# Kernel tuning notes

Measured on AMD Instinct MI355X. Metric: run time of the kernel, lower is better.

The kernel has to match this reference:

```python
import jax, jax.numpy as jnp
import numpy as np


def _dft_mats(N1, N):
    # Symmetric N1xN1 DFT / iDFT matrices and Cooley-Tukey twiddle factors.
    n = np.arange(N1)
    F = np.exp(-2j * np.pi * np.outer(n, n) / N1).astype(np.complex64)
    Finv = np.conj(F)  # inverse DFT matrix (1/N normalization folded into tw)
    tw = (np.exp(-2j * np.pi * np.outer(n, n) / N) / N).astype(np.complex64)
    twinv = np.exp(2j * np.pi * np.outer(n, n) / N).astype(np.complex64)
    return F, Finv, tw, twinv


def setup_inputs() -> dict:
    key = jax.random.key(0)
    ku, kk = jax.random.split(key)
    B, H, N = 128, 128, 1024
    u = jax.random.normal(ku, (B, H, N), dtype=jnp.float32)
    k = jax.random.normal(kk, (H, N), dtype=jnp.float32)
    return {"u": u, "k": k}


def reference(u, k):
    # Four-step (Monarch / Cooley-Tukey) FFT convolution: y = ifft(fft(u) * fft(k)).real
    # decomposed into N1xN1 complex matmuls with twiddle multiplies, matching TKFFTConv.
    B, H, N = u.shape
    N1 = int(round(np.sqrt(N)))
    F, Finv, tw, twinv = map(jnp.asarray, _dft_mats(N1, N))

    # Filter spectrum, reshaped (k2, k1) then transposed -> (H, k1, k2), as in __init__.
    kf = jnp.fft.fft(k, n=N)                              # (H, N) complex64
    kfT = jnp.swapaxes(kf.reshape(H, N1, N1), -1, -2)     # (H, k1, k2)

    x = u.reshape(B, H, N1, N1).astype(jnp.complex64)     # (B, H, n1, n2)
    x = jnp.einsum('kn,bhnm->bhkm', F, x)                 # DFT over n1 -> (k1, n2)
    x = x * tw                                            # twiddle (includes 1/N)
    x = jnp.einsum('bhkn,nl->bhkl', x, F)                 # DFT over n2 -> (k1, k2)
    x = x * kfT[None]                                     # pointwise filter in freq
    x = jnp.einsum('bhkl,ln->bhkn', x, Finv)              # iDFT over k2 -> (k1, n2)
    x = x * twinv                                         # inverse twiddle
    x = jnp.einsum('nk,bhkm->bhnm', Finv, x)              # iDFT over k1 -> (n1, n2)
    return x.real.reshape(B, H, N)
```

## Files before the change

kernel.cpp:

```cpp
#include <hip/hip_runtime.h>
#include <hip/hip_bf16.h>
#include <math.h>

typedef __attribute__((ext_vector_type(8))) short short8;
typedef __attribute__((ext_vector_type(16))) float f32x16;

union U {
    unsigned u[4];
    short8 s;
};

struct FragH {
    U f[2];
};

static __device__ __forceinline__ unsigned short f2bf(float x) {
    __bf16 b = (__bf16)x;
    return __builtin_bit_cast(unsigned short, b);
}
static __device__ __forceinline__ unsigned packbf(float a, float b) {
    return (unsigned)f2bf(a) | ((unsigned)f2bf(b) << 16);
}

#define MFMA(A, B, C) __builtin_amdgcn_mfma_f32_32x32x16_bf16((A).s, (B).s, (C), 0, 0, 0)


__global__ __launch_bounds__(256) void fft_tables(float2* tabs, uint4* Ftab) {
    int gid = blockIdx.x * 256 + threadIdx.x;
    if (gid < 1024) {
        int i = gid;
        int r = i >> 5, c = i & 31;
        float s32, c32;
        sincospif((float)((r * c) & 31) / 16.0f, &s32, &c32);
        s32 = -s32;
        tabs[i]        = make_float2(c32,  s32);
        tabs[1024 + i] = make_float2(c32, -s32);
        float sN, cN;
        sincospif((float)(r * c) / 512.0f, &sN, &cN);
        sN = -sN;
        tabs[2048 + i] = make_float2(cN / 1024.0f, sN / 1024.0f);
        tabs[3072 + i] = make_float2(cN, -sN);
    }
    if (gid < 1536) {
        int c = gid >> 9;
        int rem = gid & 511;
        int t = rem >> 8;
        int sub = rem & 255;
        int l = sub >> 2;
        int v = sub & 3;
        int k0 = 16 * t + 8 * (l >> 5) + 2 * v;
        int j = l & 31;
        unsigned short sh[2];
        for (int q = 0; q < 2; q++) {
            int k = k0 + q;
            float sa, ca;
            sincospif((float)((k * j) & 31) / 16.0f, &sa, &ca);
            float base = (c == 0) ? ca : ((c == 1) ? -sa : sa);
            sh[q] = f2bf(base);
        }
        ((unsigned*)Ftab)[((c * 2 + t) * 64 + l) * 4 + v] =
            (unsigned)sh[0] | ((unsigned)sh[1] << 16);
    }
}

__global__ __launch_bounds__(256) void kf_kernel(const float* __restrict__ kin,
                                                 const float2* __restrict__ tabs,
                                                 float2* __restrict__ kf_cd) {
    __shared__ float  sx[1024];
    __shared__ float2 sA[1024];
    const int h = blockIdx.x, t = threadIdx.x;
    for (int i = t; i < 1024; i += 256) sx[i] = kin[h * 1024 + i];
    __syncthreads();
    const int r = t >> 3, c0 = (t & 7) << 2;

    float2 acc[4];
    for (int j = 0; j < 4; j++) acc[j] = make_float2(0.f, 0.f);
    #pragma unroll 8
    for (int n1 = 0; n1 < 32; n1++) {
        float2 f = tabs[r * 32 + n1];
        for (int j = 0; j < 4; j++) {
            float xv = sx[n1 * 32 + c0 + j];
            acc[j].x += f.x * xv;
            acc[j].y += f.y * xv;
        }
    }
    for (int j = 0; j < 4; j++) {
        float2 w = tabs[3072 + r * 32 + c0 + j];
        sA[r * 32 + c0 + j] = make_float2(acc[j].x * w.x + acc[j].y * w.y,
                                          acc[j].y * w.x - acc[j].x * w.y);
    }
    __syncthreads();
    for (int j = 0; j < 4; j++) acc[j] = make_float2(0.f, 0.f);
    #pragma unroll 8
    for (int n2 = 0; n2 < 32; n2++) {
        float2 a = sA[r * 32 + n2];
        for (int j = 0; j < 4; j++) {
            float2 f = tabs[n2 * 32 + c0 + j];
            acc[j].x += a.x * f.x - a.y * f.y;
            acc[j].y += a.x * f.y + a.y * f.x;
        }
    }
    for (int j = 0; j < 4; j++) {
        int k2 = c0 + j;
        int m = (k2 & 3) | ((k2 >> 3) << 2);
        int hl = (k2 >> 2) & 1;
        kf_cd[h * 1024 + m * 64 + hl * 32 + r] =
            make_float2(acc[j].x * (1.0f / 1024.0f), acc[j].y * (1.0f / 1024.0f));
    }
}

static __device__ __forceinline__ void convertP(const f32x16& acc, FragH& out) {
    #pragma unroll
    for (int t = 0; t < 2; t++) {
        unsigned a0 = packbf(acc[8 * t + 0], acc[8 * t + 1]);
        unsigned a1 = packbf(acc[8 * t + 2], acc[8 * t + 3]);
        unsigned b0 = packbf(acc[8 * t + 4], acc[8 * t + 5]);
        unsigned b1 = packbf(acc[8 * t + 6], acc[8 * t + 7]);
        asm("v_permlane32_swap_b32 %0, %1" : "+v"(a0), "+v"(b0));
        asm("v_permlane32_swap_b32 %0, %1" : "+v"(a1), "+v"(b1));
        out.f[t].u[0] = a0;
        out.f[t].u[1] = a1;
        out.f[t].u[2] = b0;
        out.f[t].u[3] = b1;
    }
}

__global__ __launch_bounds__(256, 3) void conv_mfma(const float* __restrict__ u,
                                                    const uint4* __restrict__ Ftab,
                                                    const float2* __restrict__ KF,
                                                    float* __restrict__ out) {
    __shared__ float2 sKF[1024];

    const int tid = threadIdx.x;
    const int lane = tid & 63;
    const int wave = tid >> 6;
    const int col = lane & 31;
    const int hl = lane >> 5;
    const size_t tile_stride = (size_t)128 * 1024;

    U F[3][2];
    #pragma unroll
    for (int c = 0; c < 3; c++)
        #pragma unroll
        for (int t = 0; t < 2; t++) {
            uint4 raw = Ftab[(c * 2 + t) * 64 + lane];
            F[c][t].u[0] = raw.x; F[c][t].u[1] = raw.y;
            F[c][t].u[2] = raw.z; F[c][t].u[3] = raw.w;
        }

    float2 t1[16];
    #pragma unroll
    for (int m = 0; m < 16; m++) {
        int row = (m & 3) + 8 * (m >> 2) + 4 * hl;
        float rev = (float)(col * row) * (1.0f / 1024.0f);
        t1[m] = make_float2(__builtin_amdgcn_cosf(rev), -__builtin_amdgcn_sinf(rev));
    }

    const f32x16 Z16 = {0,0,0,0,0,0,0,0,0,0,0,0,0,0,0,0};

    for (int unit = 0; unit < 2; unit++) {
        const int pair = unit * 4096 + blockIdx.x * 4 + wave;
        const int h = pair >> 6;
        const int b0 = (pair & 63) * 2;

        if (unit) __syncthreads();
        for (int i = tid; i < 1024; i += 256)
            sKF[i] = KF[h * 1024 + i];
        __syncthreads();

        const float* upr = u + ((size_t)(b0 * 128 + h) << 10);
        const float* upi = upr + tile_stride;
        U Xr[2], Xi[2];
        #pragma unroll
        for (int t = 0; t < 2; t++) {
            float xr[8], xi[8];
            #pragma unroll
            for (int e = 0; e < 8; e++) {
                int off = (16 * t + 8 * hl + e) * 32 + col;
                xr[e] = upr[off];
                xi[e] = upi[off];
            }
            #pragma unroll
            for (int v = 0; v < 4; v++) {
                Xr[t].u[v] = packbf(xr[2 * v], xr[2 * v + 1]);
                Xi[t].u[v] = packbf(xi[2 * v], xi[2 * v + 1]);
            }
        }

        f32x16 aR = Z16, aI = Z16;
        #pragma unroll
        for (int t = 0; t < 2; t++) {
            aR = MFMA(Xr[t], F[0][t], aR); aR = MFMA(Xi[t], F[2][t], aR);
            aI = MFMA(Xr[t], F[1][t], aI); aI = MFMA(Xi[t], F[0][t], aI);
        }
        #pragma unroll
        for (int m = 0; m < 16; m++) {
            float rr = aR[m] * t1[m].x - aI[m] * t1[m].y;
            float ii = aR[m] * t1[m].y + aI[m] * t1[m].x;
            aR[m] = rr; aI[m] = ii;
        }
        FragH Yr, Yi;
        convertP(aR, Yr);
        convertP(aI, Yi);

        f32x16 bR = Z16, bI = Z16;
        #pragma unroll
        for (int t = 0; t < 2; t++) {
            bR = MFMA(F[0][t], Yr.f[t], bR); bR = MFMA(F[2][t], Yi.f[t], bR);
            bI = MFMA(F[0][t], Yi.f[t], bI); bI = MFMA(F[1][t], Yr.f[t], bI);
        }
        #pragma unroll
        for (int m = 0; m < 16; m++) {
            float2 kv = sKF[m * 64 + lane];
            float rr = bR[m] * kv.x - bI[m] * kv.y;
            float ii = bR[m] * kv.y + bI[m] * kv.x;
            bR[m] = rr; bI[m] = ii;
        }
        FragH Zr, Zi;
        convertP(bR, Zr);
        convertP(bI, Zi);

        aR = Z16; aI = Z16;
        #pragma unroll
        for (int t = 0; t < 2; t++) {
            aR = MFMA(Zr.f[t], F[0][t], aR); aR = MFMA(Zi.f[t], F[1][t], aR);
            aI = MFMA(Zr.f[t], F[2][t], aI); aI = MFMA(Zi.f[t], F[0][t], aI);
        }
        #pragma unroll
        for (int m = 0; m < 16; m++) {
            float rr = aR[m] * t1[m].x + aI[m] * t1[m].y;
            float ii = aI[m] * t1[m].x - aR[m] * t1[m].y;
            aR[m] = rr; aI[m] = ii;
        }
        FragH Wr, Wi;
        convertP(aR, Wr);
        convertP(aI, Wi);

        f32x16 yR = Z16, yI = Z16;
        #pragma unroll
        for (int t = 0; t < 2; t++) {
            yR = MFMA(F[0][t], Wr.f[t], yR); yR = MFMA(F[1][t], Wi.f[t], yR);
            yI = MFMA(F[0][t], Wi.f[t], yI); yI = MFMA(F[2][t], Wr.f[t], yI);
        }
        float* opr = out + ((size_t)(b0 * 128 + h) << 10);
        float* opi = opr + tile_stride;
        #pragma unroll
        for (int m = 0; m < 16; m++) {
            int off = ((m & 3) + 8 * (m >> 2) + 4 * hl) * 32 + col;
            opr[off] = yR[m];
            opi[off] = yI[m];
        }
    }
}

extern "C" void kernel_launch(void* const* d_in, const int* in_sizes, int n_in,
                              void* d_out, int out_size, void* d_ws, size_t ws_size,
                              hipStream_t stream) {
    const float* u = (const float*)d_in[0];
    const float* k = (const float*)d_in[1];
    float* out = (float*)d_out;

    float2* tabs  = (float2*)d_ws;
    uint4*  Ftab  = (uint4*)((char*)d_ws + 49152);
    float2* kf_cd = (float2*)((char*)d_ws + 65536);

    fft_tables<<<16, 256, 0, stream>>>(tabs, Ftab);
    kf_kernel<<<128, 256, 0, stream>>>(k, tabs, kf_cd);
    conv_mfma<<<1024, 256, 0, stream>>>(u, Ftab, kf_cd, out);
}
```

Before: 43.94 us.

## Drop per-block unit loop, stage DFT fragments in LDS, raise occupancy

Removes the two-unit loop so each block handles one pair set, and launches twice as many blocks. The DFT fragment table moves from registers into shared memory and is reloaded before each MFMA stage. Twiddles are recomputed with sin/cos in each stage instead of being held in registers. Launch bounds go from 3 to 4 blocks per CU. The aim is to cut register pressure and raise occupancy, at the cost of extra LDS reads, repeated transcendental work and a redundant per-block filter load.

```diff
diff --git a/kernel.cpp b/kernel.cpp
--- a/kernel.cpp
+++ b/kernel.cpp
@@ -125,10 +125,11 @@
     }
 }
 
-__global__ __launch_bounds__(256, 3) void conv_mfma(const float* __restrict__ u,
+__global__ __launch_bounds__(256, 4) void conv_mfma(const float* __restrict__ u,
                                                     const uint4* __restrict__ Ftab,
                                                     const float2* __restrict__ KF,
                                                     float* __restrict__ out) {
+    __shared__ uint4  sF[384];
     __shared__ float2 sKF[1024];
 
     const int tid = threadIdx.x;
@@ -138,119 +139,106 @@
     const int hl = lane >> 5;
     const size_t tile_stride = (size_t)128 * 1024;
 
-    U F[3][2];
-    #pragma unroll
-    for (int c = 0; c < 3; c++)
+    const int pair = blockIdx.x * 4 + wave;
+    const int h = blockIdx.x >> 4;
+    const int b0 = (pair & 63) * 2;
+
+    for (int i = tid; i < 384; i += 256) sF[i] = Ftab[i];
+    for (int i = tid; i < 1024; i += 256) sKF[i] = KF[h * 1024 + i];
+    __syncthreads();
+
+    const f32x16 Z16 = {0,0,0,0,0,0,0,0,0,0,0,0,0,0,0,0};
+
+    const float* upr = u + ((size_t)(b0 * 128 + h) << 10);
+    const float* upi = upr + tile_stride;
+    U Xr[2], Xi[2];
+    #pragma unroll
+    for (int t = 0; t < 2; t++) {
         #pragma unroll
-        for (int t = 0; t < 2; t++) {
-            uint4 raw = Ftab[(c * 2 + t) * 64 + lane];
-            F[c][t].u[0] = raw.x; F[c][t].u[1] = raw.y;
-            F[c][t].u[2] = raw.z; F[c][t].u[3] = raw.w;
-        }
-
-    float2 t1[16];
+        for (int v = 0; v < 4; v++) {
+            int off = (16 * t + 8 * hl + 2 * v) * 32 + col;
+            Xr[t].u[v] = packbf(upr[off], upr[off + 32]);
+            Xi[t].u[v] = packbf(upi[off], upi[off + 32]);
+        }
+    }
+
+    #define LOADF(c, t) ({ U r_; uint4 raw_ = sF[((c) * 2 + (t)) * 64 + lane]; \
+        r_.u[0] = raw_.x; r_.u[1] = raw_.y; r_.u[2] = raw_.z; r_.u[3] = raw_.w; r_; })
+
+    f32x16 aR = Z16, aI = Z16;
+    #pragma unroll
+    for (int t = 0; t < 2; t++) {
+        U F0 = LOADF(0, t), F1 = LOADF(1, t), F2 = LOADF(2, t);
+        aR = MFMA(Xr[t], F0, aR); aR = MFMA(Xi[t], F2, aR);
+        aI = MFMA(Xr[t], F1, aI); aI = MFMA(Xi[t], F0, aI);
+    }
     #pragma unroll
     for (int m = 0; m < 16; m++) {
         int row = (m & 3) + 8 * (m >> 2) + 4 * hl;
         float rev = (float)(col * row) * (1.0f / 1024.0f);
-        t1[m] = make_float2(__builtin_amdgcn_cosf(rev), -__builtin_amdgcn_sinf(rev));
-    }
-
-    const f32x16 Z16 = {0,0,0,0,0,0,0,0,0,0,0,0,0,0,0,0};
-
-    for (int unit = 0; unit < 2; unit++) {
-        const int pair = unit * 4096 + blockIdx.x * 4 + wave;
-        const int h = pair >> 6;
-        const int b0 = (pair & 63) * 2;
-
-        if (unit) __syncthreads();
-        for (int i = tid; i < 1024; i += 256)
-            sKF[i] = KF[h * 1024 + i];
-        __syncthreads();
-
-        const float* upr = u + ((size_t)(b0 * 128 + h) << 10);
-        const float* upi = upr + tile_stride;
-        U Xr[2], Xi[2];
-        #pragma unroll
-        for (int t = 0; t < 2; t++) {
-            float xr[8], xi[8];
-            #pragma unroll
-            for (int e = 0; e < 8; e++) {
-                int off = (16 * t + 8 * hl + e) * 32 + col;
-                xr[e] = upr[off];
-                xi[e] = upi[off];
-            }
-            #pragma unroll
-            for (int v = 0; v < 4; v++) {
-                Xr[t].u[v] = packbf(xr[2 * v], xr[2 * v + 1]);
-                Xi[t].u[v] = packbf(xi[2 * v], xi[2 * v + 1]);
-            }
-        }
-
-        f32x16 aR = Z16, aI = Z16;
-        #pragma unroll
-        for (int t = 0; t < 2; t++) {
-            aR = MFMA(Xr[t], F[0][t], aR); aR = MFMA(Xi[t], F[2][t], aR);
-            aI = MFMA(Xr[t], F[1][t], aI); aI = MFMA(Xi[t], F[0][t], aI);
-        }
-        #pragma unroll
-        for (int m = 0; m < 16; m++) {
-            float rr = aR[m] * t1[m].x - aI[m] * t1[m].y;
-            float ii = aR[m] * t1[m].y + aI[m] * t1[m].x;
-            aR[m] = rr; aI[m] = ii;
-        }
-        FragH Yr, Yi;
-        convertP(aR, Yr);
-        convertP(aI, Yi);
-
-        f32x16 bR = Z16, bI = Z16;
-        #pragma unroll
-        for (int t = 0; t < 2; t++) {
-            bR = MFMA(F[0][t], Yr.f[t], bR); bR = MFMA(F[2][t], Yi.f[t], bR);
-            bI = MFMA(F[0][t], Yi.f[t], bI); bI = MFMA(F[1][t], Yr.f[t], bI);
-        }
-        #pragma unroll
-        for (int m = 0; m < 16; m++) {
-            float2 kv = sKF[m * 64 + lane];
-            float rr = bR[m] * kv.x - bI[m] * kv.y;
-            float ii = bR[m] * kv.y + bI[m] * kv.x;
-            bR[m] = rr; bI[m] = ii;
-        }
-        FragH Zr, Zi;
-        convertP(bR, Zr);
-        convertP(bI, Zi);
-
-        aR = Z16; aI = Z16;
-        #pragma unroll
-        for (int t = 0; t < 2; t++) {
-            aR = MFMA(Zr.f[t], F[0][t], aR); aR = MFMA(Zi.f[t], F[1][t], aR);
-            aI = MFMA(Zr.f[t], F[2][t], aI); aI = MFMA(Zi.f[t], F[0][t], aI);
-        }
-        #pragma unroll
-        for (int m = 0; m < 16; m++) {
-            float rr = aR[m] * t1[m].x + aI[m] * t1[m].y;
-            float ii = aI[m] * t1[m].x - aR[m] * t1[m].y;
-            aR[m] = rr; aI[m] = ii;
-        }
-        FragH Wr, Wi;
-        convertP(aR, Wr);
-        convertP(aI, Wi);
-
-        f32x16 yR = Z16, yI = Z16;
-        #pragma unroll
-        for (int t = 0; t < 2; t++) {
-            yR = MFMA(F[0][t], Wr.f[t], yR); yR = MFMA(F[1][t], Wi.f[t], yR);
-            yI = MFMA(F[0][t], Wi.f[t], yI); yI = MFMA(F[2][t], Wr.f[t], yI);
-        }
-        float* opr = out + ((size_t)(b0 * 128 + h) << 10);
-        float* opi = opr + tile_stride;
-        #pragma unroll
-        for (int m = 0; m < 16; m++) {
-            int off = ((m & 3) + 8 * (m >> 2) + 4 * hl) * 32 + col;
-            opr[off] = yR[m];
-            opi[off] = yI[m];
-        }
-    }
+        float cc = __builtin_amdgcn_cosf(rev), ss = __builtin_amdgcn_sinf(rev);
+        float rr = aR[m] * cc + aI[m] * ss;
+        float ii = aI[m] * cc - aR[m] * ss;
+        aR[m] = rr; aI[m] = ii;
+    }
+    FragH Yr, Yi;
+    convertP(aR, Yr);
+    convertP(aI, Yi);
+
+    f32x16 bR = Z16, bI = Z16;
+    #pragma unroll
+    for (int t = 0; t < 2; t++) {
+        U F0 = LOADF(0, t), F1 = LOADF(1, t), F2 = LOADF(2, t);
+        bR = MFMA(F0, Yr.f[t], bR); bR = MFMA(F2, Yi.f[t], bR);
+        bI = MFMA(F0, Yi.f[t], bI); bI = MFMA(F1, Yr.f[t], bI);
+    }
+    #pragma unroll
+    for (int m = 0; m < 16; m++) {
+        float2 kv = sKF[m * 64 + lane];
+        float rr = bR[m] * kv.x - bI[m] * kv.y;
+        float ii = bR[m] * kv.y + bI[m] * kv.x;
+        bR[m] = rr; bI[m] = ii;
+    }
+    FragH Zr, Zi;
+    convertP(bR, Zr);
+    convertP(bI, Zi);
+
+    aR = Z16; aI = Z16;
+    #pragma unroll
+    for (int t = 0; t < 2; t++) {
+        U F0 = LOADF(0, t), F1 = LOADF(1, t), F2 = LOADF(2, t);
+        aR = MFMA(Zr.f[t], F0, aR); aR = MFMA(Zi.f[t], F1, aR);
+        aI = MFMA(Zr.f[t], F2, aI); aI = MFMA(Zi.f[t], F0, aI);
+    }
+    #pragma unroll
+    for (int m = 0; m < 16; m++) {
+        int row = (m & 3) + 8 * (m >> 2) + 4 * hl;
+        float rev = (float)(col * row) * (1.0f / 1024.0f);
+        float cc = __builtin_amdgcn_cosf(rev), ss = __builtin_amdgcn_sinf(rev);
+        float rr = aR[m] * cc - aI[m] * ss;
+        float ii = aI[m] * cc + aR[m] * ss;
+        aR[m] = rr; aI[m] = ii;
+    }
+    FragH Wr, Wi;
+    convertP(aR, Wr);
+    convertP(aI, Wi);
+
+    f32x16 yR = Z16, yI = Z16;
+    #pragma unroll
+    for (int t = 0; t < 2; t++) {
+        U F0 = LOADF(0, t), F1 = LOADF(1, t), F2 = LOADF(2, t);
+        yR = MFMA(F0, Wr.f[t], yR); yR = MFMA(F1, Wi.f[t], yR);
+        yI = MFMA(F0, Wi.f[t], yI); yI = MFMA(F2, Wr.f[t], yI);
+    }
+    float* opr = out + ((size_t)(b0 * 128 + h) << 10);
+    float* opi = opr + tile_stride;
+    #pragma unroll
+    for (int m = 0; m < 16; m++) {
+        int off = ((m & 3) + 8 * (m >> 2) + 4 * hl) * 32 + col;
+        opr[off] = yR[m];
+        opi[off] = yI[m];
+    }
+    #undef LOADF
 }
 
 extern "C" void kernel_launch(void* const* d_in, const int* in_sizes, int n_in,
@@ -266,5 +254,5 @@
 
     fft_tables<<<16, 256, 0, stream>>>(tabs, Ftab);
     kf_kernel<<<128, 256, 0, stream>>>(k, tabs, kf_cd);
-    conv_mfma<<<1024, 256, 0, stream>>>(u, Ftab, kf_cd, out);
-}
+    conv_mfma<<<2048, 256, 0, stream>>>(u, Ftab, kf_cd, out);
+}
```

New measurement: 48.01 us. 9.3% more time.

## Double-buffer input tiles via async global-to-LDS loads, four pairs per wave

Applied to the files above, without the earlier changes.

Each wave now processes four consecutive batch pairs for the same head. Input tiles are prefetched with global_load_lds into per-wave double-buffered LDS so the next tile's load overlaps the current tile's MFMA work. The filter spectrum is held in registers rather than reloaded into shared memory behind block barriers, and the grid is halved with launch bounds lowered to 2 blocks per CU. The cost is more LDS per block and lower occupancy, and the manual vmcnt waits rely on the store/load counter ordering being correct.

```diff
diff --git a/kernel.cpp b/kernel.cpp
--- a/kernel.cpp
+++ b/kernel.cpp
@@ -23,6 +23,12 @@
 }
 
 #define MFMA(A, B, C) __builtin_amdgcn_mfma_f32_32x32x16_bf16((A).s, (B).s, (C), 0, 0, 0)
+
+static __device__ __forceinline__ void gll16(const float* g, float* l) {
+    __builtin_amdgcn_global_load_lds(
+        (const __attribute__((address_space(1))) void*)g,
+        (__attribute__((address_space(3))) void*)l, 16, 0, 0);
+}
 
 
 __global__ __launch_bounds__(256) void fft_tables(float2* tabs, uint4* Ftab) {
@@ -125,11 +131,80 @@
     }
 }
 
-__global__ __launch_bounds__(256, 3) void conv_mfma(const float* __restrict__ u,
+static __device__ __forceinline__ void compute_pair14(
+        const U Xr[2], const U Xi[2], const U F[3][2],
+        const float2 t1[16], const float2 kf[16],
+        float* __restrict__ opr, float* __restrict__ opi,
+        int hl, int col) {
+    const f32x16 Z16 = {0,0,0,0,0,0,0,0,0,0,0,0,0,0,0,0};
+
+    f32x16 aR = Z16, aI = Z16;
+    #pragma unroll
+    for (int t = 0; t < 2; t++) {
+        aR = MFMA(Xr[t], F[0][t], aR); aR = MFMA(Xi[t], F[2][t], aR);
+        aI = MFMA(Xr[t], F[1][t], aI); aI = MFMA(Xi[t], F[0][t], aI);
+    }
+    #pragma unroll
+    for (int m = 0; m < 16; m++) {
+        float rr = aR[m] * t1[m].x - aI[m] * t1[m].y;
+        float ii = aR[m] * t1[m].y + aI[m] * t1[m].x;
+        aR[m] = rr; aI[m] = ii;
+    }
+    FragH Yr, Yi;
+    convertP(aR, Yr);
+    convertP(aI, Yi);
+
+    f32x16 bR = Z16, bI = Z16;
+    #pragma unroll
+    for (int t = 0; t < 2; t++) {
+        bR = MFMA(F[0][t], Yr.f[t], bR); bR = MFMA(F[2][t], Yi.f[t], bR);
+        bI = MFMA(F[0][t], Yi.f[t], bI); bI = MFMA(F[1][t], Yr.f[t], bI);
+    }
+    #pragma unroll
+    for (int m = 0; m < 16; m++) {
+        float rr = bR[m] * kf[m].x - bI[m] * kf[m].y;
+        float ii = bR[m] * kf[m].y + bI[m] * kf[m].x;
+        bR[m] = rr; bI[m] = ii;
+    }
+    FragH Zr, Zi;
+    convertP(bR, Zr);
+    convertP(bI, Zi);
+
+    aR = Z16; aI = Z16;
+    #pragma unroll
+    for (int t = 0; t < 2; t++) {
+        aR = MFMA(Zr.f[t], F[0][t], aR); aR = MFMA(Zi.f[t], F[1][t], aR);
+        aI = MFMA(Zr.f[t], F[2][t], aI); aI = MFMA(Zi.f[t], F[0][t], aI);
+    }
+    #pragma unroll
+    for (int m = 0; m < 16; m++) {
+        float rr = aR[m] * t1[m].x + aI[m] * t1[m].y;
+        float ii = aI[m] * t1[m].x - aR[m] * t1[m].y;
+        aR[m] = rr; aI[m] = ii;
+    }
+    FragH Wr, Wi;
+    convertP(aR, Wr);
+    convertP(aI, Wi);
+
+    f32x16 yR = Z16, yI = Z16;
+    #pragma unroll
+    for (int t = 0; t < 2; t++) {
+        yR = MFMA(F[0][t], Wr.f[t], yR); yR = MFMA(F[1][t], Wi.f[t], yR);
+        yI = MFMA(F[0][t], Wi.f[t], yI); yI = MFMA(F[2][t], Wr.f[t], yI);
+    }
+    #pragma unroll
+    for (int m = 0; m < 16; m++) {
+        int off = ((m & 3) + 8 * (m >> 2) + 4 * hl) * 32 + col;
+        opr[off] = yR[m];
+        opi[off] = yI[m];
+    }
+}
+
+__global__ __launch_bounds__(256, 2) void conv_mfma(const float* __restrict__ u,
                                                     const uint4* __restrict__ Ftab,
                                                     const float2* __restrict__ KF,
                                                     float* __restrict__ out) {
-    __shared__ float2 sKF[1024];
+    __shared__ float sBuf[4][2][2048];
 
     const int tid = threadIdx.x;
     const int lane = tid & 63;
@@ -137,6 +212,9 @@
     const int col = lane & 31;
     const int hl = lane >> 5;
     const size_t tile_stride = (size_t)128 * 1024;
+
+    const int p0 = blockIdx.x * 16 + wave * 4;
+    const int h = p0 >> 6;
 
     U F[3][2];
     #pragma unroll
@@ -147,7 +225,9 @@
             F[c][t].u[0] = raw.x; F[c][t].u[1] = raw.y;
             F[c][t].u[2] = raw.z; F[c][t].u[3] = raw.w;
         }
-
+    float2 kf[16];
+    #pragma unroll
+    for (int m = 0; m < 16; m++) kf[m] = KF[h * 1024 + m * 64 + lane];
     float2 t1[16];
     #pragma unroll
     for (int m = 0; m < 16; m++) {
@@ -155,102 +235,65 @@
         float rev = (float)(col * row) * (1.0f / 1024.0f);
         t1[m] = make_float2(__builtin_amdgcn_cosf(rev), -__builtin_amdgcn_sinf(rev));
     }
-
-    const f32x16 Z16 = {0,0,0,0,0,0,0,0,0,0,0,0,0,0,0,0};
-
-    for (int unit = 0; unit < 2; unit++) {
-        const int pair = unit * 4096 + blockIdx.x * 4 + wave;
-        const int h = pair >> 6;
-        const int b0 = (pair & 63) * 2;
-
-        if (unit) __syncthreads();
-        for (int i = tid; i < 1024; i += 256)
-            sKF[i] = KF[h * 1024 + i];
-        __syncthreads();
-
-        const float* upr = u + ((size_t)(b0 * 128 + h) << 10);
-        const float* upi = upr + tile_stride;
-        U Xr[2], Xi[2];
-        #pragma unroll
-        for (int t = 0; t < 2; t++) {
-            float xr[8], xi[8];
-            #pragma unroll
-            for (int e = 0; e < 8; e++) {
-                int off = (16 * t + 8 * hl + e) * 32 + col;
-                xr[e] = upr[off];
-                xi[e] = upi[off];
-            }
-            #pragma unroll
-            for (int v = 0; v < 4; v++) {
-                Xr[t].u[v] = packbf(xr[2 * v], xr[2 * v + 1]);
-                Xi[t].u[v] = packbf(xi[2 * v], xi[2 * v + 1]);
-            }
-        }
-
-        f32x16 aR = Z16, aI = Z16;
-        #pragma unroll
-        for (int t = 0; t < 2; t++) {
-            aR = MFMA(Xr[t], F[0][t], aR); aR = MFMA(Xi[t], F[2][t], aR);
-            aI = MFMA(Xr[t], F[1][t], aI); aI = MFMA(Xi[t], F[0][t], aI);
-        }
-        #pragma unroll
-        for (int m = 0; m < 16; m++) {
-            float rr = aR[m] * t1[m].x - aI[m] * t1[m].y;
-            float ii = aR[m] * t1[m].y + aI[m] * t1[m].x;
-            aR[m] = rr; aI[m] = ii;
-        }
-        FragH Yr, Yi;
-        convertP(aR, Yr);
-        convertP(aI, Yi);
-
-        f32x16 bR = Z16, bI = Z16;
-        #pragma unroll
-        for (int t = 0; t < 2; t++) {
-            bR = MFMA(F[0][t], Yr.f[t], bR); bR = MFMA(F[2][t], Yi.f[t], bR);
-            bI = MFMA(F[0][t], Yi.f[t], bI); bI = MFMA(F[1][t], Yr.f[t], bI);
-        }
-        #pragma unroll
-        for (int m = 0; m < 16; m++) {
-            float2 kv = sKF[m * 64 + lane];
-            float rr = bR[m] * kv.x - bI[m] * kv.y;
-            float ii = bR[m] * kv.y + bI[m] * kv.x;
-            bR[m] = rr; bI[m] = ii;
-        }
-        FragH Zr, Zi;
-        convertP(bR, Zr);
-        convertP(bI, Zi);
-
-        aR = Z16; aI = Z16;
-        #pragma unroll
-        for (int t = 0; t < 2; t++) {
-            aR = MFMA(Zr.f[t], F[0][t], aR); aR = MFMA(Zi.f[t], F[1][t], aR);
-            aI = MFMA(Zr.f[t], F[2][t], aI); aI = MFMA(Zi.f[t], F[0][t], aI);
-        }
-        #pragma unroll
-        for (int m = 0; m < 16; m++) {
-            float rr = aR[m] * t1[m].x + aI[m] * t1[m].y;
-            float ii = aI[m] * t1[m].x - aR[m] * t1[m].y;
-            aR[m] = rr; aI[m] = ii;
-        }
-        FragH Wr, Wi;
-        convertP(aR, Wr);
-        convertP(aI, Wi);
-
-        f32x16 yR = Z16, yI = Z16;
-        #pragma unroll
-        for (int t = 0; t < 2; t++) {
-            yR = MFMA(F[0][t], Wr.f[t], yR); yR = MFMA(F[1][t], Wi.f[t], yR);
-            yI = MFMA(F[0][t], Wi.f[t], yI); yI = MFMA(F[2][t], Wr.f[t], yI);
-        }
-        float* opr = out + ((size_t)(b0 * 128 + h) << 10);
-        float* opi = opr + tile_stride;
-        #pragma unroll
-        for (int m = 0; m < 16; m++) {
-            int off = ((m & 3) + 8 * (m >> 2) + 4 * hl) * 32 + col;
-            opr[off] = yR[m];
-            opi[off] = yI[m];
-        }
-    }
+    asm volatile("s_waitcnt vmcnt(0)" ::: "memory");
+
+    float* bufA = &sBuf[wave][0][0];
+    float* bufB = &sBuf[wave][1][0];
+
+    #define STAGE(j, buf) do {                                                \
+        int b0_ = ((p0 + (j)) & 63) * 2;                                      \
+        const float* sR_ = u + ((size_t)(b0_ * 128 + h) << 10);               \
+        const float* sI_ = sR_ + tile_stride;                                 \
+        _Pragma("unroll")                                                     \
+        for (int c_ = 0; c_ < 4; c_++) {                                      \
+            gll16(sR_ + c_ * 256 + lane * 4, (buf) + c_ * 256);               \
+            gll16(sI_ + c_ * 256 + lane * 4, (buf) + 1024 + c_ * 256);        \
+        }                                                                     \
+    } while (0)
+
+    #define FRAGS(buf, Xr, Xi) do {                                           \
+        _Pragma("unroll")                                                     \
+        for (int t_ = 0; t_ < 2; t_++)                                        \
+            _Pragma("unroll")                                                 \
+            for (int v_ = 0; v_ < 4; v_++) {                                  \
+                int r0_ = (16 * t_ + 8 * hl + 2 * v_) * 32 + col;             \
+                (Xr)[t_].u[v_] = packbf((buf)[r0_], (buf)[r0_ + 32]);         \
+                (Xi)[t_].u[v_] = packbf((buf)[1024 + r0_], (buf)[1024 + r0_ + 32]); \
+            }                                                                 \
+    } while (0)
+
+    #define OUTP(j) (out + ((size_t)((((p0 + (j)) & 63) * 2) * 128 + h) << 10))
+
+    U Xr[2], Xi[2];
+
+    STAGE(0, bufA);
+    STAGE(1, bufB);
+
+    asm volatile("s_waitcnt vmcnt(8)" ::: "memory");
+    FRAGS(bufA, Xr, Xi);
+    asm volatile("s_waitcnt lgkmcnt(0)" ::: "memory");
+    __builtin_amdgcn_sched_barrier(0);
+    STAGE(2, bufA);
+    { float* o = OUTP(0); compute_pair14(Xr, Xi, F, t1, kf, o, o + tile_stride, hl, col); }
+
+    asm volatile("s_waitcnt vmcnt(8)" ::: "memory");
+    FRAGS(bufB, Xr, Xi);
+    asm volatile("s_waitcnt lgkmcnt(0)" ::: "memory");
+    __builtin_amdgcn_sched_barrier(0);
+    STAGE(3, bufB);
+    { float* o = OUTP(1); compute_pair14(Xr, Xi, F, t1, kf, o, o + tile_stride, hl, col); }
+
+    asm volatile("s_waitcnt vmcnt(8)" ::: "memory");
+    FRAGS(bufA, Xr, Xi);
+    { float* o = OUTP(2); compute_pair14(Xr, Xi, F, t1, kf, o, o + tile_stride, hl, col); }
+
+    asm volatile("s_waitcnt vmcnt(0)" ::: "memory");
+    FRAGS(bufB, Xr, Xi);
+    { float* o = OUTP(3); compute_pair14(Xr, Xi, F, t1, kf, o, o + tile_stride, hl, col); }
+
+    #undef STAGE
+    #undef FRAGS
+    #undef OUTP
 }
 
 extern "C" void kernel_launch(void* const* d_in, const int* in_sizes, int n_in,
@@ -266,5 +309,5 @@
 
     fft_tables<<<16, 256, 0, stream>>>(tabs, Ftab);
     kf_kernel<<<128, 256, 0, stream>>>(k, tabs, kf_cd);
-    conv_mfma<<<1024, 256, 0, stream>>>(u, Ftab, kf_cd, out);
-}
+    conv_mfma<<<512, 256, 0, stream>>>(u, Ftab, kf_cd, out);
+}
```

Result: no change. 43.75 us (-0.4%).
